# Performance work log

Measured on AMD Instinct MI355X. Metric: run time of the kernel, lower is better.

## Reference

```python
import jax, jax.numpy as jnp
import numpy as np

EPS = 1e-5  # eqx.nn.LayerNorm default


def _layer_norm(x, w, b):
    m = x.mean(-1, keepdims=True)
    v = ((x - m) ** 2).mean(-1, keepdims=True)
    return (x - m) / jnp.sqrt(v + EPS) * w + b


def _s4_block(x, nw, nb, lre, lim, bre, bim, cre, cim, d, lstep, ow, ob, o2w, o2b):
    # x: [L, H]. One SequenceBlock: LayerNorm -> S4 recurrence (lax.scan) -> GELU -> GLU-style gated linear -> residual.
    skip = x
    h = _layer_norm(x, nw, nb)
    Lam = lre + 1j * lim                      # [H, N] complex diagonal state matrix
    step = jnp.exp(lstep)[:, None]            # [H, 1] per-channel timescale
    BL = 1.0 / (1.0 - (step / 2.0) * Lam)     # bilinear discretization
    Abar = BL * (1.0 + (step / 2.0) * Lam)    # [H, N]
    Bbar = BL * step * (bre + 1j * bim)       # [H, N]
    C = cre + 1j * cim                        # [H, N]

    def scan_fn(state, u):                    # state: [H, N] complex, u: [H]
        new = Abar * state + Bbar * u[:, None]
        y = 2.0 * jnp.sum(C * new, axis=-1).real + d * u
        return new, y

    init = jnp.zeros(Abar.shape, Abar.dtype)  # cell.init_state
    _, y = jax.lax.scan(scan_fn, init, h)     # [L, H]
    y = jax.nn.gelu(y)
    y = (y @ ow.T + ob) * jax.nn.sigmoid(y @ o2w.T + o2b)
    return skip + y


def setup_inputs() -> dict:
    key = jax.random.key(0)
    L, IN, OUT, H, N, NL = 2048, 4, 3, 512, 32, 4
    ks = jax.random.split(key, 16)
    return {
        "x": jax.random.normal(ks[0], (L, IN), jnp.float32),
        "enc_w": jax.random.normal(ks[1], (H, IN), jnp.float32) / np.sqrt(IN),
        "enc_b": jnp.zeros((H,), jnp.float32),
        "dec_w": jax.random.normal(ks[2], (OUT, H), jnp.float32) / np.sqrt(H),
        "dec_b": jnp.zeros((OUT,), jnp.float32),
        "norm_w": jnp.ones((NL, H), jnp.float32),
        "norm_b": jnp.zeros((NL, H), jnp.float32),
        "lam_re": -0.5 - jax.random.uniform(ks[3], (NL, H, N), jnp.float32),  # stable (Re < 0)
        "lam_im": np.pi * jax.random.normal(ks[4], (NL, H, N), jnp.float32),
        "b_re": jax.random.normal(ks[5], (NL, H, N), jnp.float32) / np.sqrt(N),
        "b_im": jax.random.normal(ks[6], (NL, H, N), jnp.float32) / np.sqrt(N),
        "c_re": jax.random.normal(ks[7], (NL, H, N), jnp.float32) / np.sqrt(N),
        "c_im": jax.random.normal(ks[8], (NL, H, N), jnp.float32) / np.sqrt(N),
        "d": jax.random.normal(ks[9], (NL, H), jnp.float32),
        "log_step": float(np.log(1e-3)) + float(np.log(1e-1) - np.log(1e-3)) * jax.random.uniform(ks[10], (NL, H), jnp.float32),
        "out_w": jax.random.normal(ks[11], (NL, H, H), jnp.float32) / np.sqrt(H),
        "out_b": jnp.zeros((NL, H), jnp.float32),
        "out2_w": jax.random.normal(ks[12], (NL, H, H), jnp.float32) / np.sqrt(H),
        "out2_b": jnp.zeros((NL, H), jnp.float32),
    }


def reference(x, enc_w, enc_b, dec_w, dec_b, norm_w, norm_b, lam_re, lam_im, b_re, b_im, c_re, c_im, d, log_step, out_w, out_b, out2_w, out2_b):
    h = x @ enc_w.T + enc_b                   # encoder: [L, IN] -> [L, H]
    for i in range(norm_w.shape[0]):          # fixed small n_layers loop
        h = _s4_block(h, norm_w[i], norm_b[i], lam_re[i], lam_im[i], b_re[i], b_im[i],
                      c_re[i], c_im[i], d[i], log_step[i], out_w[i], out_b[i], out2_w[i], out2_b[i])
    return h @ dec_w.T + dec_b                # decoder: [L, H] -> [L, OUT]
```

## Files before the change

### kernel.cpp

```cpp
#include <hip/hip_runtime.h>
#include <hip/hip_bf16.h>
#include <math.h>

#define LSEQ 2048
#define HD   512
#define NST  32
#define LC   16
#define NCHK 128
#define SUP  16
#define NSUP 8
#define HH   (HD * HD)

typedef __bf16 bf16;
typedef __bf16 bf16x8 __attribute__((ext_vector_type(8)));
typedef float  floatx4 __attribute__((ext_vector_type(4)));

__device__ __forceinline__ float wave_reduce_add(float v) {
#pragma unroll
    for (int m = 32; m; m >>= 1) v += __shfl_xor(v, m, 64);
    return v;
}

__device__ __forceinline__ float gelu_tanh(float x) {
    float z = 0.7978845608028654f * (x + 0.044715f * x * x * x);
    float e = __expf(2.f * z);
    float th = 1.f - 2.f / (e + 1.f);
    return 0.5f * x * (1.f + th);
}

__device__ __forceinline__ void make_ab(float lre, float lim, float step,
                                        float br0, float bi0,
                                        float& ar, float& ai, float& br, float& bi) {
    float s2 = 0.5f * step;
    float dr = 1.f - s2 * lre, di = -s2 * lim;
    float inv = 1.f / (dr * dr + di * di);
    float blr = dr * inv, bli = -di * inv;
    float nr = 1.f + s2 * lre, ni = s2 * lim;
    ar = blr * nr - bli * ni;
    ai = blr * ni + bli * nr;
    float tr = step * br0, ti = step * bi0;
    br = blr * tr - bli * ti;
    bi = blr * ti + bli * tr;
}

__global__ __launch_bounds__(256) void prep_kernel(
    const float* __restrict__ lre, const float* __restrict__ lim,
    const float* __restrict__ bre, const float* __restrict__ bim,
    const float* __restrict__ cre, const float* __restrict__ cim,
    const float* __restrict__ ls,
    float2* __restrict__ cA, float2* __restrict__ cB,
    float2* __restrict__ cC, float2* __restrict__ cAp) {
    int tid = blockIdx.x * 256 + threadIdx.x;
    int lay = tid >> 14, rem = tid & 16383;
    int ch = rem >> 5, n = rem & 31;
    int src = tid;
    float step = __expf(ls[lay * HD + ch]);
    float ar, ai, br, bi;
    make_ab(lre[src], lim[src], step, bre[src], bim[src], ar, ai, br, bi);
    float xr = ar, xi = ai;
#pragma unroll
    for (int q = 0; q < 4; ++q) { float tt = xr * xr - xi * xi; xi = 2.f * xr * xi; xr = tt; }
    int dst = (lay * NST + n) * HD + ch;
    cA[dst]  = make_float2(ar, ai);
    cB[dst]  = make_float2(br, bi);
    cC[dst]  = make_float2(2.f * cre[src], 2.f * cim[src]);
    cAp[dst] = make_float2(xr, xi);
}

__global__ __launch_bounds__(256) void cvt_kernel(
    const float* __restrict__ ow, const float* __restrict__ o2w,
    bf16* __restrict__ wb) {
    const float* src = blockIdx.y ? o2w : ow;
    bf16* dst = wb + blockIdx.y * (4 * HH);
    int i = (blockIdx.x * 256 + threadIdx.x) * 8;
    float4 a = *(const float4*)(src + i);
    float4 b = *(const float4*)(src + i + 4);
    bf16x8 o;
    o[0] = (bf16)a.x; o[1] = (bf16)a.y; o[2] = (bf16)a.z; o[3] = (bf16)a.w;
    o[4] = (bf16)b.x; o[5] = (bf16)b.y; o[6] = (bf16)b.z; o[7] = (bf16)b.w;
    *(bf16x8*)(dst + i) = o;
}

__global__ __launch_bounds__(256) void enc_kernel(
    const float* __restrict__ x, const float* __restrict__ w,
    const float* __restrict__ b, float* __restrict__ h) {
    int idx = blockIdx.x * 256 + threadIdx.x;
    int t = idx >> 9, i = idx & (HD - 1);
    float acc = b[i];
    float4 xv = *(const float4*)(x + t * 4);
    float4 wv = *(const float4*)(w + i * 4);
    acc = fmaf(xv.x, wv.x, acc);
    acc = fmaf(xv.y, wv.y, acc);
    acc = fmaf(xv.z, wv.z, acc);
    acc = fmaf(xv.w, wv.w, acc);
    h[idx] = acc;
}

__global__ __launch_bounds__(256) void ln_kernel(
    const float* __restrict__ h, float* __restrict__ hn,
    const float* __restrict__ w, const float* __restrict__ b) {
    int wv = threadIdx.x >> 6, lane = threadIdx.x & 63;
    int row = blockIdx.x * 4 + wv;
    const float* hp = h + row * HD + lane * 8;
    float v[8];
    *(float4*)(v)     = *(const float4*)(hp);
    *(float4*)(v + 4) = *(const float4*)(hp + 4);
    float s = 0.f;
#pragma unroll
    for (int e = 0; e < 8; ++e) s += v[e];
    s = wave_reduce_add(s);
    float m = s * (1.f / HD);
    float q = 0.f;
#pragma unroll
    for (int e = 0; e < 8; ++e) { float d = v[e] - m; q += d * d; }
    q = wave_reduce_add(q);
    float rstd = rsqrtf(q * (1.f / HD) + 1e-5f);
    float w8[8], b8[8];
    *(float4*)(w8)     = *(const float4*)(w + lane * 8);
    *(float4*)(w8 + 4) = *(const float4*)(w + lane * 8 + 4);
    *(float4*)(b8)     = *(const float4*)(b + lane * 8);
    *(float4*)(b8 + 4) = *(const float4*)(b + lane * 8 + 4);
    float o[8];
#pragma unroll
    for (int e = 0; e < 8; ++e)
        o[e] = (v[e] - m) * rstd * w8[e] + b8[e];
    float* op = hn + row * HD + lane * 8;
    *(float4*)op       = *(float4*)o;
    *(float4*)(op + 4) = *(float4*)(o + 4);
}

__global__ __launch_bounds__(256, 4) void p1_kernel(
    const float* __restrict__ u,
    const float2* __restrict__ cA, const float2* __restrict__ cB,
    float2* __restrict__ f, int lay) {
    int lane = threadIdx.x & 63, w = threadIdx.x >> 6;
    int ch = blockIdx.x * 16 + (lane & 15);
    int sub = lane >> 4;
    int chunk = blockIdx.y * 4 + w;
    int cbase = (lay * NST + sub * 8) * HD + ch;
    float aR[8], aI[8], bR[8], bI[8];
#pragma unroll
    for (int j = 0; j < 8; ++j) {
        float2 t = cA[cbase + j * HD]; aR[j] = t.x; aI[j] = t.y;
        t = cB[cbase + j * HD];        bR[j] = t.x; bI[j] = t.y;
    }
    float sr[8], si[8];
#pragma unroll
    for (int j = 0; j < 8; ++j) { sr[j] = 0.f; si[j] = 0.f; }
    const float* up = u + chunk * LC * HD + ch;
#pragma unroll 4
    for (int t = 0; t < LC; ++t) {
        float uu = up[t * HD];
#pragma unroll
        for (int j = 0; j < 8; ++j) {
            float nr = fmaf(aR[j], sr[j], fmaf(-aI[j], si[j], bR[j] * uu));
            float ni = fmaf(aI[j], sr[j], fmaf( aR[j], si[j], bI[j] * uu));
            sr[j] = nr; si[j] = ni;
        }
    }
    float2* fp = f + (chunk * NST + sub * 8) * HD + ch;
#pragma unroll
    for (int j = 0; j < 8; ++j) fp[j * HD] = make_float2(sr[j], si[j]);
}

__global__ __launch_bounds__(256) void p2a_kernel(
    float2* __restrict__ f, const float2* __restrict__ cAp, int lay) {
    int tg = blockIdx.x * 256 + threadIdx.x;
    int ch = tg & 511;
    int ns = tg >> 9;
    int n = ns & 31, sup = ns >> 5;
    float2 ap = cAp[(lay * NST + n) * HD + ch];
    float2* fp = f + ((sup * SUP) * NST + n) * HD + ch;
    float sr = 0.f, si = 0.f;
#pragma unroll 4
    for (int j = 0; j < SUP; ++j) {
        float2 v = fp[(size_t)j * NST * HD];
        float nr = fmaf(ap.x, sr, fmaf(-ap.y, si, v.x));
        float ni = fmaf(ap.y, sr, fmaf( ap.x, si, v.y));
        sr = nr; si = ni;
        fp[(size_t)j * NST * HD] = make_float2(sr, si);
    }
}

__global__ __launch_bounds__(256) void p2b_kernel(
    float2* __restrict__ f, const float2* __restrict__ cAp, int lay) {
    int tg = blockIdx.x * 256 + threadIdx.x;
    int ch = tg & 511, n = tg >> 9;
    float2 ap = cAp[(lay * NST + n) * HD + ch];
    float xr = ap.x, xi = ap.y;
#pragma unroll
    for (int q = 0; q < 4; ++q) { float tt = xr * xr - xi * xi; xi = 2.f * xr * xi; xr = tt; }
    float2* fp = f + ((SUP - 1) * NST + n) * HD + ch;
    const size_t stride = (size_t)SUP * NST * HD;
    float sr = 0.f, si = 0.f;
#pragma unroll
    for (int k = 0; k < NSUP; ++k) {
        float2 v = fp[k * stride];
        float nr = fmaf(xr, sr, fmaf(-xi, si, v.x));
        float ni = fmaf(xi, sr, fmaf( xr, si, v.y));
        sr = nr; si = ni;
        fp[k * stride] = make_float2(sr, si);
    }
}

__global__ __launch_bounds__(256) void p2c_kernel(
    float2* __restrict__ f, const float2* __restrict__ cAp, int lay) {
    int tg = blockIdx.x * 256 + threadIdx.x;
    int ch = tg & 511;
    int ns = tg >> 9;
    int n = ns & 31, sup = ns >> 5;
    if (sup == 0) return;
    float2 ap = cAp[(lay * NST + n) * HD + ch];
    float2 S = f[((sup * SUP - 1) * NST + n) * HD + ch];
    float2* fp = f + ((sup * SUP) * NST + n) * HD + ch;
    float wr = ap.x, wi = ap.y;
#pragma unroll 4
    for (int j = 0; j < SUP - 1; ++j) {
        float2 v = fp[(size_t)j * NST * HD];
        v.x += wr * S.x - wi * S.y;
        v.y += wr * S.y + wi * S.x;
        fp[(size_t)j * NST * HD] = v;
        float nwr = wr * ap.x - wi * ap.y;
        float nwi = wr * ap.y + wi * ap.x;
        wr = nwr; wi = nwi;
    }
}

__global__ __launch_bounds__(256, 3) void p3_kernel(
    const float* __restrict__ u, const float2* __restrict__ f,
    const float2* __restrict__ cA, const float2* __restrict__ cB,
    const float2* __restrict__ cC, const float* __restrict__ d_p,
    bf16* __restrict__ g, int lay) {
    int lane = threadIdx.x & 63, w = threadIdx.x >> 6;
    int ch = blockIdx.x * 16 + (lane & 15);
    int sub = lane >> 4;
    int chunk = blockIdx.y * 4 + w;
    int cbase = (lay * NST + sub * 8) * HD + ch;
    float aR[8], aI[8], bR[8], bI[8], cR[8], cI[8];
#pragma unroll
    for (int j = 0; j < 8; ++j) {
        float2 t = cA[cbase + j * HD]; aR[j] = t.x; aI[j] = t.y;
        t = cB[cbase + j * HD];        bR[j] = t.x; bI[j] = t.y;
        t = cC[cbase + j * HD];        cR[j] = t.x; cI[j] = t.y;
    }
    float dch = d_p[lay * HD + ch];
    float sr[8], si[8];
    if (chunk > 0) {
        const float2* ip = f + ((chunk - 1) * NST + sub * 8) * HD + ch;
#pragma unroll
        for (int j = 0; j < 8; ++j) { float2 v = ip[j * HD]; sr[j] = v.x; si[j] = v.y; }
    } else {
#pragma unroll
        for (int j = 0; j < 8; ++j) { sr[j] = 0.f; si[j] = 0.f; }
    }
    const float* up = u + chunk * LC * HD + ch;
    bf16* gp = g + chunk * LC * HD + ch;
#pragma unroll 4
    for (int t = 0; t < LC; ++t) {
        float uu = up[t * HD];
        float p = 0.f;
#pragma unroll
        for (int j = 0; j < 8; ++j) {
            float nr = fmaf(aR[j], sr[j], fmaf(-aI[j], si[j], bR[j] * uu));
            float ni = fmaf(aI[j], sr[j], fmaf( aR[j], si[j], bI[j] * uu));
            sr[j] = nr; si[j] = ni;
            p = fmaf(cR[j], nr, fmaf(-cI[j], ni, p));
        }
        p += __shfl_xor(p, 16);
        p += __shfl_xor(p, 32);
        float y = fmaf(dch, uu, p);
        if (sub == 0) gp[t * HD] = (bf16)gelu_tanh(y);
    }
}

__global__ __launch_bounds__(256) void mm_kernel(
    const bf16* __restrict__ A,
    const bf16* __restrict__ W1,
    const bf16* __restrict__ W2,
    const float* __restrict__ bias1, const float* __restrict__ bias2,
    float* __restrict__ Hio) {
    const int w = threadIdx.x >> 6, lane = threadIdx.x & 63;
    const int wm = w >> 1, wn = w & 1;
    const int mBase = blockIdx.y * 64 + wm * 32;
    const int nBase = blockIdx.x * 64 + wn * 32;
    const int lrow = lane & 15, quad = lane >> 4;

    floatx4 acc1[2][2] = {{{0.f,0.f,0.f,0.f},{0.f,0.f,0.f,0.f}},{{0.f,0.f,0.f,0.f},{0.f,0.f,0.f,0.f}}};
    floatx4 acc2[2][2] = {{{0.f,0.f,0.f,0.f},{0.f,0.f,0.f,0.f}},{{0.f,0.f,0.f,0.f},{0.f,0.f,0.f,0.f}}};

    for (int k0 = 0; k0 < HD; k0 += 32) {
        int kk = k0 + quad * 8;
        bf16x8 a0 = *(const bf16x8*)(A + (mBase + lrow) * HD + kk);
        bf16x8 a1 = *(const bf16x8*)(A + (mBase + 16 + lrow) * HD + kk);
        bf16x8 p0 = *(const bf16x8*)(W1 + (nBase + lrow) * HD + kk);
        bf16x8 p1 = *(const bf16x8*)(W1 + (nBase + 16 + lrow) * HD + kk);
        bf16x8 q0 = *(const bf16x8*)(W2 + (nBase + lrow) * HD + kk);
        bf16x8 q1 = *(const bf16x8*)(W2 + (nBase + 16 + lrow) * HD + kk);
        acc1[0][0] = __builtin_amdgcn_mfma_f32_16x16x32_bf16(a0, p0, acc1[0][0], 0, 0, 0);
        acc1[0][1] = __builtin_amdgcn_mfma_f32_16x16x32_bf16(a0, p1, acc1[0][1], 0, 0, 0);
        acc1[1][0] = __builtin_amdgcn_mfma_f32_16x16x32_bf16(a1, p0, acc1[1][0], 0, 0, 0);
        acc1[1][1] = __builtin_amdgcn_mfma_f32_16x16x32_bf16(a1, p1, acc1[1][1], 0, 0, 0);
        acc2[0][0] = __builtin_amdgcn_mfma_f32_16x16x32_bf16(a0, q0, acc2[0][0], 0, 0, 0);
        acc2[0][1] = __builtin_amdgcn_mfma_f32_16x16x32_bf16(a0, q1, acc2[0][1], 0, 0, 0);
        acc2[1][0] = __builtin_amdgcn_mfma_f32_16x16x32_bf16(a1, q0, acc2[1][0], 0, 0, 0);
        acc2[1][1] = __builtin_amdgcn_mfma_f32_16x16x32_bf16(a1, q1, acc2[1][1], 0, 0, 0);
    }

#pragma unroll
    for (int fm = 0; fm < 2; ++fm)
#pragma unroll
        for (int fn = 0; fn < 2; ++fn) {
            int j = nBase + fn * 16 + lrow;
            float bb1 = bias1[j], bb2 = bias2[j];
#pragma unroll
            for (int r = 0; r < 4; ++r) {
                int t = mBase + fm * 16 + quad * 4 + r;
                float z1 = acc1[fm][fn][r] + bb1;
                float z2 = acc2[fm][fn][r] + bb2;
                float val = z1 / (1.f + __expf(-z2));
                Hio[t * HD + j] += val;
            }
        }
}

__global__ __launch_bounds__(192) void dec_kernel(
    const float* __restrict__ h, const float* __restrict__ w,
    const float* __restrict__ b, float* __restrict__ out) {
    int j = threadIdx.x >> 6, lane = threadIdx.x & 63;
    int t = blockIdx.x;
    const float* hp = h + t * HD + lane * 8;
    float v[8];
    *(float4*)(v)     = *(const float4*)(hp);
    *(float4*)(v + 4) = *(const float4*)(hp + 4);
    float w8[8];
    *(float4*)(w8)     = *(const float4*)(w + j * HD + lane * 8);
    *(float4*)(w8 + 4) = *(const float4*)(w + j * HD + lane * 8 + 4);
    float s = 0.f;
#pragma unroll
    for (int e = 0; e < 8; ++e) s = fmaf(v[e], w8[e], s);
    s = wave_reduce_add(s);
    if (lane == 0) out[t * 3 + j] = s + b[j];
}

extern "C" void kernel_launch(void* const* d_in, const int* in_sizes, int n_in,
                              void* d_out, int out_size, void* d_ws, size_t ws_size,
                              hipStream_t stream) {
    const float* x   = (const float*)d_in[0];
    const float* ew  = (const float*)d_in[1];
    const float* eb  = (const float*)d_in[2];
    const float* dw  = (const float*)d_in[3];
    const float* db  = (const float*)d_in[4];
    const float* nw  = (const float*)d_in[5];
    const float* nb  = (const float*)d_in[6];
    const float* lre = (const float*)d_in[7];
    const float* lim = (const float*)d_in[8];
    const float* bre = (const float*)d_in[9];
    const float* bim = (const float*)d_in[10];
    const float* cre = (const float*)d_in[11];
    const float* cim = (const float*)d_in[12];
    const float* dd  = (const float*)d_in[13];
    const float* ls  = (const float*)d_in[14];
    const float* ow  = (const float*)d_in[15];
    const float* ob  = (const float*)d_in[16];
    const float* o2w = (const float*)d_in[17];
    const float* o2b = (const float*)d_in[18];

    char* ws = (char*)d_ws;
    float*  h   = (float*)ws;
    float*  hn  = (float*)(ws + (4  << 20));
    float2* f   = (float2*)(ws + (8  << 20));
    bf16*   g   = (bf16*)(ws + (24 << 20));
    bf16*   wb  = (bf16*)(ws + (26 << 20));
    float2* cA  = (float2*)(ws + (30 << 20));
    float2* cB  = (float2*)(ws + (30 << 20) + (512 << 10));
    float2* cC  = (float2*)(ws + (31 << 20));
    float2* cAp = (float2*)(ws + (31 << 20) + (512 << 10));

    prep_kernel<<<256, 256, 0, stream>>>(lre, lim, bre, bim, cre, cim, ls, cA, cB, cC, cAp);
    cvt_kernel<<<dim3(4 * HH / (256 * 8), 2), 256, 0, stream>>>(ow, o2w, wb);
    enc_kernel<<<LSEQ * HD / 256, 256, 0, stream>>>(x, ew, eb, h);
    for (int lay = 0; lay < 4; ++lay) {
        int oH = lay * HD;
        ln_kernel<<<LSEQ / 4, 256, 0, stream>>>(h, hn, nw + oH, nb + oH);
        p1_kernel<<<dim3(HD / 16, NCHK / 4), 256, 0, stream>>>(hn, cA, cB, f, lay);
        p2a_kernel<<<512, 256, 0, stream>>>(f, cAp, lay);
        p2b_kernel<<<64, 256, 0, stream>>>(f, cAp, lay);
        p2c_kernel<<<512, 256, 0, stream>>>(f, cAp, lay);
        p3_kernel<<<dim3(HD / 16, NCHK / 4), 256, 0, stream>>>(hn, f, cA, cB, cC, dd, g, lay);
        mm_kernel<<<dim3(HD / 64, LSEQ / 64), 256, 0, stream>>>(
            g, wb + lay * HH, wb + 4 * HH + lay * HH, ob + oH, o2b + oH, h);
    }
    dec_kernel<<<LSEQ, 192, 0, stream>>>(h, dw, db, (float*)d_out);
}
```

Before: 343.1 us.

## Double scan chunk length and stage input tiles in shared memory

```diff
diff --git a/kernel.cpp b/kernel.cpp
--- a/kernel.cpp
+++ b/kernel.cpp
@@ -5,9 +5,9 @@
 #define LSEQ 2048
 #define HD   512
 #define NST  32
-#define LC   16
-#define NCHK 128
-#define SUP  16
+#define LC   32
+#define NCHK 64
+#define SUP  8
 #define NSUP 8
 #define HH   (HD * HD)
 
@@ -59,7 +59,7 @@
     make_ab(lre[src], lim[src], step, bre[src], bim[src], ar, ai, br, bi);
     float xr = ar, xi = ai;
 #pragma unroll
-    for (int q = 0; q < 4; ++q) { float tt = xr * xr - xi * xi; xi = 2.f * xr * xi; xr = tt; }
+    for (int q = 0; q < 5; ++q) { float tt = xr * xr - xi * xi; xi = 2.f * xr * xi; xr = tt; }
     int dst = (lay * NST + n) * HD + ch;
     cA[dst]  = make_float2(ar, ai);
     cB[dst]  = make_float2(br, bi);
@@ -129,14 +129,24 @@
     *(float4*)(op + 4) = *(float4*)(o + 4);
 }
 
-__global__ __launch_bounds__(256, 4) void p1_kernel(
+__global__ __launch_bounds__(256, 2) void p1_kernel(
     const float* __restrict__ u,
     const float2* __restrict__ cA, const float2* __restrict__ cB,
     float2* __restrict__ f, int lay) {
-    int lane = threadIdx.x & 63, w = threadIdx.x >> 6;
-    int ch = blockIdx.x * 16 + (lane & 15);
+    __shared__ float tile[4 * LC * 16];
+    int tid = threadIdx.x;
+    int lane = tid & 63, w = tid >> 6;
+    int chl = lane & 15;
+    int ch = blockIdx.x * 16 + chl;
     int sub = lane >> 4;
     int chunk = blockIdx.y * 4 + w;
+    int t0 = blockIdx.y * 4 * LC;
+    const float* ub = u + (size_t)t0 * HD + blockIdx.x * 16;
+#pragma unroll
+    for (int r = 0; r < 8; ++r) {
+        int idx = r * 256 + tid;
+        tile[idx] = ub[(idx >> 4) * HD + (idx & 15)];
+    }
     int cbase = (lay * NST + sub * 8) * HD + ch;
     float aR[8], aI[8], bR[8], bI[8];
 #pragma unroll
@@ -147,10 +157,11 @@
     float sr[8], si[8];
 #pragma unroll
     for (int j = 0; j < 8; ++j) { sr[j] = 0.f; si[j] = 0.f; }
-    const float* up = u + chunk * LC * HD + ch;
+    __syncthreads();
+    const float* tp = tile + (w * LC) * 16 + chl;
 #pragma unroll 4
     for (int t = 0; t < LC; ++t) {
-        float uu = up[t * HD];
+        float uu = tp[t * 16];
 #pragma unroll
         for (int j = 0; j < 8; ++j) {
             float nr = fmaf(aR[j], sr[j], fmaf(-aI[j], si[j], bR[j] * uu));
@@ -172,7 +183,7 @@
     float2 ap = cAp[(lay * NST + n) * HD + ch];
     float2* fp = f + ((sup * SUP) * NST + n) * HD + ch;
     float sr = 0.f, si = 0.f;
-#pragma unroll 4
+#pragma unroll
     for (int j = 0; j < SUP; ++j) {
         float2 v = fp[(size_t)j * NST * HD];
         float nr = fmaf(ap.x, sr, fmaf(-ap.y, si, v.x));
@@ -189,7 +200,7 @@
     float2 ap = cAp[(lay * NST + n) * HD + ch];
     float xr = ap.x, xi = ap.y;
 #pragma unroll
-    for (int q = 0; q < 4; ++q) { float tt = xr * xr - xi * xi; xi = 2.f * xr * xi; xr = tt; }
+    for (int q = 0; q < 3; ++q) { float tt = xr * xr - xi * xi; xi = 2.f * xr * xi; xr = tt; }
     float2* fp = f + ((SUP - 1) * NST + n) * HD + ch;
     const size_t stride = (size_t)SUP * NST * HD;
     float sr = 0.f, si = 0.f;
@@ -214,7 +225,7 @@
     float2 S = f[((sup * SUP - 1) * NST + n) * HD + ch];
     float2* fp = f + ((sup * SUP) * NST + n) * HD + ch;
     float wr = ap.x, wi = ap.y;
-#pragma unroll 4
+#pragma unroll
     for (int j = 0; j < SUP - 1; ++j) {
         float2 v = fp[(size_t)j * NST * HD];
         v.x += wr * S.x - wi * S.y;
@@ -226,15 +237,25 @@
     }
 }
 
-__global__ __launch_bounds__(256, 3) void p3_kernel(
+__global__ __launch_bounds__(256, 2) void p3_kernel(
     const float* __restrict__ u, const float2* __restrict__ f,
     const float2* __restrict__ cA, const float2* __restrict__ cB,
     const float2* __restrict__ cC, const float* __restrict__ d_p,
     bf16* __restrict__ g, int lay) {
-    int lane = threadIdx.x & 63, w = threadIdx.x >> 6;
-    int ch = blockIdx.x * 16 + (lane & 15);
+    __shared__ float tile[4 * LC * 16];
+    int tid = threadIdx.x;
+    int lane = tid & 63, w = tid >> 6;
+    int chl = lane & 15;
+    int ch = blockIdx.x * 16 + chl;
     int sub = lane >> 4;
     int chunk = blockIdx.y * 4 + w;
+    int t0 = blockIdx.y * 4 * LC;
+    const float* ub = u + (size_t)t0 * HD + blockIdx.x * 16;
+#pragma unroll
+    for (int r = 0; r < 8; ++r) {
+        int idx = r * 256 + tid;
+        tile[idx] = ub[(idx >> 4) * HD + (idx & 15)];
+    }
     int cbase = (lay * NST + sub * 8) * HD + ch;
     float aR[8], aI[8], bR[8], bI[8], cR[8], cI[8];
 #pragma unroll
@@ -253,11 +274,12 @@
 #pragma unroll
         for (int j = 0; j < 8; ++j) { sr[j] = 0.f; si[j] = 0.f; }
     }
-    const float* up = u + chunk * LC * HD + ch;
-    bf16* gp = g + chunk * LC * HD + ch;
+    __syncthreads();
+    const float* tp = tile + (w * LC) * 16 + chl;
+    bf16* gp = g + (size_t)chunk * LC * HD + ch;
 #pragma unroll 4
     for (int t = 0; t < LC; ++t) {
-        float uu = up[t * HD];
+        float uu = tp[t * 16];
         float p = 0.f;
 #pragma unroll
         for (int j = 0; j < 8; ++j) {
```

Result: faster. 315.2 us (-8.2%).
